# Kernel optimization log

Hardware: AMD Instinct MI355X
Metric: run time of the kernel (lower is better)

Reference implementation:

```python
import jax, jax.numpy as jnp
import numpy as np

N_NODES = 100000
N_EDGES = 1600000
IN_DIM, HID_DIM, OUT_DIM = 256, 64, 64


def gcn_conv(x, W, b, row, col, ew):
    """PyG GCNConv: linear transform, add self-loops (weight 1), symmetric
    deg^{-1/2} normalization, gather-scale-scatter_add aggregation, bias."""
    n = x.shape[0]
    x = x @ W  # [N, out]
    loops = jnp.arange(n)
    row_f = jnp.concatenate([row, loops])
    col_f = jnp.concatenate([col, loops])
    ew_f = jnp.concatenate([ew, jnp.ones((n,), x.dtype)])
    deg = jax.ops.segment_sum(ew_f, col_f, num_segments=n)  # [N]
    dinv = jnp.where(deg > 0, jax.lax.rsqrt(deg), jnp.zeros_like(deg))
    norm = dinv[row_f] * ew_f * dinv[col_f]  # [E+N]
    msg = x[row_f] * norm[:, None]  # gather + scale, [E+N, out]
    out = jax.ops.segment_sum(msg, col_f, num_segments=n)  # scatter-add
    return out + b


def setup_inputs() -> dict:
    key = jax.random.key(0)
    k1, k2, k3, k4, k5 = jax.random.split(key, 5)
    x = jax.random.normal(k1, (N_NODES, IN_DIM), dtype=jnp.float32)
    edge_index = jax.random.randint(k2, (2, N_EDGES), 0, N_NODES, dtype=jnp.int64)
    edge_count = jax.random.randint(k3, (N_EDGES, 1), 0, 1000, dtype=jnp.int64)
    W1 = jax.random.normal(k4, (IN_DIM, HID_DIM), dtype=jnp.float32) * (1.0 / np.sqrt(IN_DIM))
    b1 = jnp.zeros((HID_DIM,), jnp.float32)
    W2 = jax.random.normal(k5, (HID_DIM, OUT_DIM), dtype=jnp.float32) * (1.0 / np.sqrt(HID_DIM))
    b2 = jnp.zeros((OUT_DIM,), jnp.float32)
    return {"x": x, "edge_index": edge_index, "edge_count": edge_count,
            "W1": W1, "b1": b1, "W2": W2, "b2": b2}


def reference(x, edge_index, edge_count, W1, b1, W2, b2):
    # edge weight: min-max normalize edge_count (squeezed)
    ec = edge_count[:, 0].astype(jnp.float32)
    ew = (ec - ec.min()) / (ec.max() - ec.min())
    row, col = edge_index[0], edge_index[1]
    h = jax.nn.relu(gcn_conv(x, W1, b1, row, col, ew))
    h = gcn_conv(h, W2, b2, row, col, ew)
    # dropout(p=0.5) is identity in eval mode
    node_embeddings = h
    return node_embeddings, jax.nn.log_softmax(h, axis=-1)
```

## Files before the change

### kernel.cpp

```cpp
#include <hip/hip_runtime.h>
#include <climits>

#define CNT_SHIFT 20
#define SUM_MASK  ((1u << 20) - 1)
#define ROW_BITS 17
#define ROW_MASK ((1u << ROW_BITS) - 1)
#define MAXDEG 64
#define HIST_ILP 4

__device__ __forceinline__ unsigned short f2bf(float f) {
  unsigned u = __float_as_uint(f);
  u = (u + 0x7fffu + ((u >> 16) & 1u)) >> 16;
  return (unsigned short)u;
}
__device__ __forceinline__ float bf_lo(unsigned d) { return __uint_as_float(d << 16); }
__device__ __forceinline__ float bf_hi(unsigned d) { return __uint_as_float(d & 0xffff0000u); }

__device__ __forceinline__ void gload16(const float* g, float* l) {
  __builtin_amdgcn_global_load_lds(
      (const __attribute__((address_space(1))) void*)(g),
      (__attribute__((address_space(3))) void*)(l),
      16, 0, 0);
}

__global__ __launch_bounds__(256) void k_mega(
    const float* __restrict__ A, const float* __restrict__ W,
    unsigned short* __restrict__ outh, int nN,
    const int* __restrict__ erow, const int* __restrict__ ecol,
    const int* __restrict__ ec,
    unsigned* __restrict__ packed, unsigned* __restrict__ srcw2,
    int* __restrict__ mm, int nE, int Bg, int S, int stride) {
  __shared__ float atile[128 * 32];
  __shared__ float wtile[32 * 64];
  __shared__ int sred[8];
  const int bid = blockIdx.x;
  const bool slot = (bid % S) == 0;
  const int kq = bid / S;

  if (slot && kq < Bg) {
    constexpr int K = 256, KSTEPS = K / 32;
    const int tid = threadIdx.x;
    const int wv = tid >> 6;
    const int tr = tid >> 4, tc = tid & 15;
    const int rbase = kq * 128;

    float4 acc[8];
    #pragma unroll
    for (int i = 0; i < 8; ++i) acc[i] = make_float4(0.f, 0.f, 0.f, 0.f);

    for (int kt = 0; kt < KSTEPS; ++kt) {
      #pragma unroll
      for (int r = 0; r < 4; ++r) {
        int f = r * 256 + tid;
        int row = f >> 3, c4s = f & 7;
        int c4 = c4s ^ (row & 7);
        int gr = rbase + row; if (gr >= nN) gr = nN - 1;
        gload16(A + (size_t)gr * K + kt * 32 + c4 * 4,
                &atile[(r * 256 + wv * 64) * 4]);
      }
      #pragma unroll
      for (int r = 0; r < 2; ++r) {
        int f = r * 256 + tid;
        int krow = f >> 4, c4 = f & 15;
        gload16(W + (size_t)(kt * 32 + krow) * 64 + c4 * 4,
                &wtile[(r * 256 + wv * 64) * 4]);
      }
      __syncthreads();
      #pragma unroll
      for (int k4 = 0; k4 < 8; ++k4) {
        float4 wv0 = *(const float4*)&wtile[(k4 * 4 + 0) * 64 + tc * 4];
        float4 wv1 = *(const float4*)&wtile[(k4 * 4 + 1) * 64 + tc * 4];
        float4 wv2 = *(const float4*)&wtile[(k4 * 4 + 2) * 64 + tc * 4];
        float4 wv3 = *(const float4*)&wtile[(k4 * 4 + 3) * 64 + tc * 4];
        #pragma unroll
        for (int i = 0; i < 8; ++i) {
          int row = tr + 16 * i;
          float4 av = *(const float4*)&atile[row * 32 + ((k4 ^ (row & 7)) * 4)];
          acc[i].x = fmaf(av.x, wv0.x, acc[i].x);
          acc[i].y = fmaf(av.x, wv0.y, acc[i].y);
          acc[i].z = fmaf(av.x, wv0.z, acc[i].z);
          acc[i].w = fmaf(av.x, wv0.w, acc[i].w);
          acc[i].x = fmaf(av.y, wv1.x, acc[i].x);
          acc[i].y = fmaf(av.y, wv1.y, acc[i].y);
          acc[i].z = fmaf(av.y, wv1.z, acc[i].z);
          acc[i].w = fmaf(av.y, wv1.w, acc[i].w);
          acc[i].x = fmaf(av.z, wv2.x, acc[i].x);
          acc[i].y = fmaf(av.z, wv2.y, acc[i].y);
          acc[i].z = fmaf(av.z, wv2.z, acc[i].z);
          acc[i].w = fmaf(av.z, wv2.w, acc[i].w);
          acc[i].x = fmaf(av.w, wv3.x, acc[i].x);
          acc[i].y = fmaf(av.w, wv3.y, acc[i].y);
          acc[i].z = fmaf(av.w, wv3.z, acc[i].z);
          acc[i].w = fmaf(av.w, wv3.w, acc[i].w);
        }
      }
      __syncthreads();
    }
    #pragma unroll
    for (int i = 0; i < 8; ++i) {
      int row = rbase + tr + 16 * i;
      if (row < nN) {
        ushort4 o4;
        o4.x = f2bf(acc[i].x); o4.y = f2bf(acc[i].y);
        o4.z = f2bf(acc[i].z); o4.w = f2bf(acc[i].w);
        *(ushort4*)&outh[(size_t)row * 64 + tc * 4] = o4;
      }
    }
    return;
  }

  int ng = slot ? min(kq, Bg) : min(kq + 1, Bg);
  int h = bid - ng;
  int gid = h * 256 + threadIdx.x;
  int vmin = INT_MAX, vmax = INT_MIN;
  #pragma unroll
  for (int k = 0; k < HIST_ILP; ++k) {
    int e = gid + k * stride;
    if (e < nE) {
      int w = ec[e];
      int c = ecol[e];
      vmin = min(vmin, w); vmax = max(vmax, w);
      unsigned old = atomicAdd(&packed[c], (1u << CNT_SHIFT) | (unsigned)w);
      int rk = (int)(old >> CNT_SHIFT); if (rk > MAXDEG - 1) rk = MAXDEG - 1;
      srcw2[(size_t)c * MAXDEG + rk] = (unsigned)erow[e] | ((unsigned)w << ROW_BITS);
    }
  }
  #pragma unroll
  for (int o = 32; o > 0; o >>= 1) {
    vmin = min(vmin, __shfl_xor(vmin, o));
    vmax = max(vmax, __shfl_xor(vmax, o));
  }
  int wid = threadIdx.x >> 6;
  if ((threadIdx.x & 63) == 0) { sred[wid] = vmin; sred[4 + wid] = vmax; }
  __syncthreads();
  if (threadIdx.x == 0) {
    #pragma unroll
    for (int w2 = 1; w2 < 4; ++w2) {
      vmin = min(vmin, sred[w2]);
      vmax = max(vmax, sred[4 + w2]);
    }
    if (vmin != INT_MAX) atomicMax(&mm[0], 0x7FFFFFFF - vmin);
    if (vmax != INT_MIN) atomicMax(&mm[1], vmax);
  }
}

__global__ void k_dinv(const unsigned* __restrict__ packed,
                       const int* __restrict__ mm,
                       float* __restrict__ dinv, int n) {
  int i = blockIdx.x * blockDim.x + threadIdx.x;
  if (i >= n) return;
  unsigned pk = packed[i];
  int v = (int)(pk >> CNT_SHIFT);
  float mn = (float)(0x7FFFFFFF - mm[0]);
  float rcp = 1.0f / ((float)mm[1] - mn);
  float deg = ((float)(pk & SUM_MASK) - (float)v * mn) * rcp;
  dinv[i] = rsqrtf(deg + 1.0f);
}

__global__ __launch_bounds__(256) void k_gemm64(const float* __restrict__ A,
                                                const float* __restrict__ W,
                                                unsigned short* __restrict__ outh,
                                                int n) {
  constexpr int K = 64, KSTEPS = K / 32;
  __shared__ float atile[2][128 * 32];
  __shared__ float wtile[2][32 * 64];
  const int tid = threadIdx.x;
  const int wv = tid >> 6;
  const int tr = tid >> 4, tc = tid & 15;
  const int rbase = blockIdx.x * 128;

  auto stageA = [&](int kt, int b) {
    #pragma unroll
    for (int r = 0; r < 4; ++r) {
      int f = r * 256 + tid;
      int row = f >> 3, c4s = f & 7;
      int c4 = c4s ^ (row & 7);
      int gr = rbase + row; if (gr >= n) gr = n - 1;
      gload16(A + (size_t)gr * K + kt * 32 + c4 * 4,
              &atile[b][(r * 256 + wv * 64) * 4]);
    }
  };
  auto stageW = [&](int kt, int b) {
    #pragma unroll
    for (int r = 0; r < 2; ++r) {
      int f = r * 256 + tid;
      int krow = f >> 4, c4 = f & 15;
      gload16(W + (size_t)(kt * 32 + krow) * 64 + c4 * 4,
              &wtile[b][(r * 256 + wv * 64) * 4]);
    }
  };

  float4 acc[8];
  #pragma unroll
  for (int i = 0; i < 8; ++i) acc[i] = make_float4(0.f, 0.f, 0.f, 0.f);

  stageA(0, 0); stageW(0, 0);
  __syncthreads();
  int cur = 0;
  for (int kt = 0; kt < KSTEPS; ++kt) {
    if (kt + 1 < KSTEPS) { stageA(kt + 1, cur ^ 1); stageW(kt + 1, cur ^ 1); }
    const float* ab = atile[cur];
    const float* wb = wtile[cur];
    #pragma unroll
    for (int k4 = 0; k4 < 8; ++k4) {
      float4 wv0 = *(const float4*)&wb[(k4 * 4 + 0) * 64 + tc * 4];
      float4 wv1 = *(const float4*)&wb[(k4 * 4 + 1) * 64 + tc * 4];
      float4 wv2 = *(const float4*)&wb[(k4 * 4 + 2) * 64 + tc * 4];
      float4 wv3 = *(const float4*)&wb[(k4 * 4 + 3) * 64 + tc * 4];
      #pragma unroll
      for (int i = 0; i < 8; ++i) {
        int row = tr + 16 * i;
        float4 av = *(const float4*)&ab[row * 32 + ((k4 ^ (row & 7)) * 4)];
        acc[i].x = fmaf(av.x, wv0.x, acc[i].x);
        acc[i].y = fmaf(av.x, wv0.y, acc[i].y);
        acc[i].z = fmaf(av.x, wv0.z, acc[i].z);
        acc[i].w = fmaf(av.x, wv0.w, acc[i].w);
        acc[i].x = fmaf(av.y, wv1.x, acc[i].x);
        acc[i].y = fmaf(av.y, wv1.y, acc[i].y);
        acc[i].z = fmaf(av.y, wv1.z, acc[i].z);
        acc[i].w = fmaf(av.y, wv1.w, acc[i].w);
        acc[i].x = fmaf(av.z, wv2.x, acc[i].x);
        acc[i].y = fmaf(av.z, wv2.y, acc[i].y);
        acc[i].z = fmaf(av.z, wv2.z, acc[i].z);
        acc[i].w = fmaf(av.z, wv2.w, acc[i].w);
        acc[i].x = fmaf(av.w, wv3.x, acc[i].x);
        acc[i].y = fmaf(av.w, wv3.y, acc[i].y);
        acc[i].z = fmaf(av.w, wv3.z, acc[i].z);
        acc[i].w = fmaf(av.w, wv3.w, acc[i].w);
      }
    }
    __syncthreads();
    cur ^= 1;
  }
  #pragma unroll
  for (int i = 0; i < 8; ++i) {
    int row = rbase + tr + 16 * i;
    if (row < n) {
      ushort4 o4;
      o4.x = f2bf(acc[i].x); o4.y = f2bf(acc[i].y);
      o4.z = f2bf(acc[i].z); o4.w = f2bf(acc[i].w);
      *(ushort4*)&outh[(size_t)row * 64 + tc * 4] = o4;
    }
  }
}

template<bool FINAL>
__global__ void k_agg(const unsigned* __restrict__ packed,
                      const unsigned* __restrict__ srcw2,
                      const int* __restrict__ mm,
                      const float* __restrict__ dinv,
                      const unsigned short* __restrict__ xwh,
                      const float* __restrict__ b,
                      float* __restrict__ outp, int nN) {
  int node = blockIdx.x * (blockDim.x >> 6) + (threadIdx.x >> 6);
  if (node >= nN) return;
  int lane = threadIdx.x & 63;
  int grp = lane >> 3, sub = lane & 7;
  float mn = (float)(0x7FFFFFFF - mm[0]);
  float rcp = 1.0f / ((float)mm[1] - mn);
  float dc = dinv[node];
  const uint4* xw16 = (const uint4*)xwh;
  float acc[8] = {0.f, 0.f, 0.f, 0.f, 0.f, 0.f, 0.f, 0.f};
  size_t s = (size_t)node * MAXDEG;
  int m = min((int)(packed[node] >> CNT_SHIFT), MAXDEG);
  {
    int take = m;
    int rsrc = 0;
    float nrmv = 0.f;
    if (lane < take) {
      unsigned rw = srcw2[s + lane];
      rsrc = rw & ROW_MASK;
      nrmv = dinv[rsrc] * (((float)(rw >> ROW_BITS) - mn) * rcp) * dc;
    }
    for (int j = 0; j < take; j += 8) {
      int jj = j + grp;
      int r = __shfl(rsrc, jj);
      float nv = __shfl(nrmv, jj);
      uint4 d = xw16[(size_t)r * 8 + sub];
      acc[0] = fmaf(nv, bf_lo(d.x), acc[0]);
      acc[1] = fmaf(nv, bf_hi(d.x), acc[1]);
      acc[2] = fmaf(nv, bf_lo(d.y), acc[2]);
      acc[3] = fmaf(nv, bf_hi(d.y), acc[3]);
      acc[4] = fmaf(nv, bf_lo(d.z), acc[4]);
      acc[5] = fmaf(nv, bf_hi(d.z), acc[5]);
      acc[6] = fmaf(nv, bf_lo(d.w), acc[6]);
      acc[7] = fmaf(nv, bf_hi(d.w), acc[7]);
    }
  }
  #pragma unroll
  for (int k = 0; k < 8; ++k) acc[k] += __shfl_xor(acc[k], 8);
  #pragma unroll
  for (int k = 0; k < 8; ++k) acc[k] += __shfl_xor(acc[k], 16);
  #pragma unroll
  for (int k = 0; k < 8; ++k) acc[k] += __shfl_xor(acc[k], 32);

  if (lane < 8) {
    uint4 d = xw16[(size_t)node * 8 + sub];
    float sv[8] = {bf_lo(d.x), bf_hi(d.x), bf_lo(d.y), bf_hi(d.y),
                   bf_lo(d.z), bf_hi(d.z), bf_lo(d.w), bf_hi(d.w)};
    float dcc = dc * dc;
    float v[8];
    #pragma unroll
    for (int k = 0; k < 8; ++k) v[k] = acc[k] + dcc * sv[k] + b[sub * 8 + k];
    size_t o0 = (size_t)node * 64 + sub * 8;
    if (FINAL) {
      *(float4*)&outp[o0]     = make_float4(v[0], v[1], v[2], v[3]);
      *(float4*)&outp[o0 + 4] = make_float4(v[4], v[5], v[6], v[7]);
      float mx = v[0];
      #pragma unroll
      for (int k = 1; k < 8; ++k) mx = fmaxf(mx, v[k]);
      #pragma unroll
      for (int o = 1; o < 8; o <<= 1) mx = fmaxf(mx, __shfl_xor(mx, o));
      float e = 0.f;
      #pragma unroll
      for (int k = 0; k < 8; ++k) e += expf(v[k] - mx);
      #pragma unroll
      for (int o = 1; o < 8; o <<= 1) e += __shfl_xor(e, o);
      float ls = mx + logf(e);
      size_t o1 = (size_t)nN * 64 + o0;
      *(float4*)&outp[o1]     = make_float4(v[0] - ls, v[1] - ls, v[2] - ls, v[3] - ls);
      *(float4*)&outp[o1 + 4] = make_float4(v[4] - ls, v[5] - ls, v[6] - ls, v[7] - ls);
    } else {
      #pragma unroll
      for (int k = 0; k < 8; ++k) v[k] = fmaxf(v[k], 0.f);
      *(float4*)&outp[o0]     = make_float4(v[0], v[1], v[2], v[3]);
      *(float4*)&outp[o0 + 4] = make_float4(v[4], v[5], v[6], v[7]);
    }
  }
}

extern "C" void kernel_launch(void* const* d_in, const int* in_sizes, int n_in,
                              void* d_out, int out_size, void* d_ws, size_t ws_size,
                              hipStream_t stream) {
  const float* x  = (const float*)d_in[0];
  const int*   ei = (const int*)d_in[1];
  const int*   ec = (const int*)d_in[2];
  const float* W1 = (const float*)d_in[3];
  const float* b1 = (const float*)d_in[4];
  const float* W2 = (const float*)d_in[5];
  const float* b2 = (const float*)d_in[6];

  int nN = in_sizes[0] / 256;
  int nE = in_sizes[2];
  const int* erow = ei;
  const int* ecol = ei + nE;
  int n64 = nN * 64;

  auto al4 = [](size_t v) { return (v + 3) & ~(size_t)3; };
  int* wsi = (int*)d_ws;
  int* mm = wsi;
  size_t off = 16;
  unsigned* packed = (unsigned*)(wsi + off);          off = al4(off + (size_t)nN);
  float* dinv   = (float*)(wsi + off);                off = al4(off + nN);
  unsigned* srcw2 = (unsigned*)(wsi + off);           off = al4(off + (size_t)MAXDEG * nN);
  unsigned short* xwh = (unsigned short*)(wsi + off); off = al4(off + 32 * (size_t)nN);
  float* h1     = (float*)(wsi + off);                off = al4(off + (size_t)n64);
  float* outp   = (float*)d_out;

  hipMemsetAsync(d_ws, 0, (size_t)(16 + nN) * 4, stream);

  int Bg = (nN + 127) / 128;
  int Bh = (nE + 256 * HIST_ILP - 1) / (256 * HIST_ILP);
  int T  = Bg + Bh;
  int S  = T / Bg; if (S < 1) S = 1;
  k_mega<<<T, 256, 0, stream>>>(x, W1, xwh, nN, erow, ecol, ec, packed, srcw2,
                                mm, nE, Bg, S, Bh * 256);
  k_dinv<<<(nN + 255) / 256, 256, 0, stream>>>(packed, mm, dinv, nN);

  k_agg<false><<<(nN + 3) / 4, 256, 0, stream>>>(packed, srcw2, mm, dinv, xwh, b1, h1, nN);

  k_gemm64<<<Bg, 256, 0, stream>>>(h1, W2, xwh, nN);
  k_agg<true><<<(nN + 3) / 4, 256, 0, stream>>>(packed, srcw2, mm, dinv, xwh, b2, outp, nN);
}
```

Measured before the change: 243.7 us.

## Fuse layer-1 aggregation with layer-2 GEMM, dropping the h1 round trip

New measurement: 288.1 us. 18.2% more time.

```diff
diff --git a/kernel.cpp b/kernel.cpp
--- a/kernel.cpp
+++ b/kernel.cpp
@@ -157,101 +157,97 @@
   dinv[i] = rsqrtf(deg + 1.0f);
 }
 
-__global__ __launch_bounds__(256) void k_gemm64(const float* __restrict__ A,
-                                                const float* __restrict__ W,
-                                                unsigned short* __restrict__ outh,
-                                                int n) {
-  constexpr int K = 64, KSTEPS = K / 32;
-  __shared__ float atile[2][128 * 32];
-  __shared__ float wtile[2][32 * 64];
-  const int tid = threadIdx.x;
-  const int wv = tid >> 6;
-  const int tr = tid >> 4, tc = tid & 15;
-  const int rbase = blockIdx.x * 128;
-
-  auto stageA = [&](int kt, int b) {
-    #pragma unroll
-    for (int r = 0; r < 4; ++r) {
-      int f = r * 256 + tid;
-      int row = f >> 3, c4s = f & 7;
-      int c4 = c4s ^ (row & 7);
-      int gr = rbase + row; if (gr >= n) gr = n - 1;
-      gload16(A + (size_t)gr * K + kt * 32 + c4 * 4,
-              &atile[b][(r * 256 + wv * 64) * 4]);
-    }
-  };
-  auto stageW = [&](int kt, int b) {
-    #pragma unroll
-    for (int r = 0; r < 2; ++r) {
-      int f = r * 256 + tid;
-      int krow = f >> 4, c4 = f & 15;
-      gload16(W + (size_t)(kt * 32 + krow) * 64 + c4 * 4,
-              &wtile[b][(r * 256 + wv * 64) * 4]);
-    }
-  };
-
-  float4 acc[8];
-  #pragma unroll
-  for (int i = 0; i < 8; ++i) acc[i] = make_float4(0.f, 0.f, 0.f, 0.f);
-
-  stageA(0, 0); stageW(0, 0);
+__global__ __launch_bounds__(256) void k_aggg(
+    const unsigned* __restrict__ packed,
+    const unsigned* __restrict__ srcw2,
+    const int* __restrict__ mm,
+    const float* __restrict__ dinv,
+    const unsigned short* __restrict__ xwh,
+    const float* __restrict__ b1,
+    const float* __restrict__ W2,
+    unsigned short* __restrict__ outh,
+    int nN) {
+  __shared__ float wlds[64 * 64];
+  {
+    const float4* W4 = (const float4*)W2;
+    float4* wl4 = (float4*)wlds;
+    for (int i = threadIdx.x; i < 1024; i += 256) wl4[i] = W4[i];
+  }
   __syncthreads();
-  int cur = 0;
-  for (int kt = 0; kt < KSTEPS; ++kt) {
-    if (kt + 1 < KSTEPS) { stageA(kt + 1, cur ^ 1); stageW(kt + 1, cur ^ 1); }
-    const float* ab = atile[cur];
-    const float* wb = wtile[cur];
-    #pragma unroll
-    for (int k4 = 0; k4 < 8; ++k4) {
-      float4 wv0 = *(const float4*)&wb[(k4 * 4 + 0) * 64 + tc * 4];
-      float4 wv1 = *(const float4*)&wb[(k4 * 4 + 1) * 64 + tc * 4];
-      float4 wv2 = *(const float4*)&wb[(k4 * 4 + 2) * 64 + tc * 4];
-      float4 wv3 = *(const float4*)&wb[(k4 * 4 + 3) * 64 + tc * 4];
-      #pragma unroll
-      for (int i = 0; i < 8; ++i) {
-        int row = tr + 16 * i;
-        float4 av = *(const float4*)&ab[row * 32 + ((k4 ^ (row & 7)) * 4)];
-        acc[i].x = fmaf(av.x, wv0.x, acc[i].x);
-        acc[i].y = fmaf(av.x, wv0.y, acc[i].y);
-        acc[i].z = fmaf(av.x, wv0.z, acc[i].z);
-        acc[i].w = fmaf(av.x, wv0.w, acc[i].w);
-        acc[i].x = fmaf(av.y, wv1.x, acc[i].x);
-        acc[i].y = fmaf(av.y, wv1.y, acc[i].y);
-        acc[i].z = fmaf(av.y, wv1.z, acc[i].z);
-        acc[i].w = fmaf(av.y, wv1.w, acc[i].w);
-        acc[i].x = fmaf(av.z, wv2.x, acc[i].x);
-        acc[i].y = fmaf(av.z, wv2.y, acc[i].y);
-        acc[i].z = fmaf(av.z, wv2.z, acc[i].z);
-        acc[i].w = fmaf(av.z, wv2.w, acc[i].w);
-        acc[i].x = fmaf(av.w, wv3.x, acc[i].x);
-        acc[i].y = fmaf(av.w, wv3.y, acc[i].y);
-        acc[i].z = fmaf(av.w, wv3.z, acc[i].z);
-        acc[i].w = fmaf(av.w, wv3.w, acc[i].w);
-      }
-    }
-    __syncthreads();
-    cur ^= 1;
-  }
-  #pragma unroll
-  for (int i = 0; i < 8; ++i) {
-    int row = rbase + tr + 16 * i;
-    if (row < n) {
-      ushort4 o4;
-      o4.x = f2bf(acc[i].x); o4.y = f2bf(acc[i].y);
-      o4.z = f2bf(acc[i].z); o4.w = f2bf(acc[i].w);
-      *(ushort4*)&outh[(size_t)row * 64 + tc * 4] = o4;
-    }
-  }
-}
-
-template<bool FINAL>
-__global__ void k_agg(const unsigned* __restrict__ packed,
-                      const unsigned* __restrict__ srcw2,
-                      const int* __restrict__ mm,
-                      const float* __restrict__ dinv,
-                      const unsigned short* __restrict__ xwh,
-                      const float* __restrict__ b,
-                      float* __restrict__ outp, int nN) {
+  int wid = threadIdx.x >> 6, lane = threadIdx.x & 63;
+  int grp = lane >> 3, sub = lane & 7;
+  float mn = (float)(0x7FFFFFFF - mm[0]);
+  float rcp = 1.0f / ((float)mm[1] - mn);
+  const uint4* xw16 = (const uint4*)xwh;
+  float4 bv0 = ((const float4*)b1)[sub * 2];
+  float4 bv1 = ((const float4*)b1)[sub * 2 + 1];
+
+  for (int it = 0; it < 4; ++it) {
+    int node = blockIdx.x * 16 + it * 4 + wid;
+    if (node >= nN) return;
+    float dc = dinv[node];
+    float acc[8] = {0.f, 0.f, 0.f, 0.f, 0.f, 0.f, 0.f, 0.f};
+    size_t s = (size_t)node * MAXDEG;
+    int m = min((int)(packed[node] >> CNT_SHIFT), MAXDEG);
+    {
+      int rsrc = 0;
+      float nrmv = 0.f;
+      if (lane < m) {
+        unsigned rw = srcw2[s + lane];
+        rsrc = rw & ROW_MASK;
+        nrmv = dinv[rsrc] * (((float)(rw >> ROW_BITS) - mn) * rcp) * dc;
+      }
+      for (int j = 0; j < m; j += 8) {
+        int jj = j + grp;
+        int r = __shfl(rsrc, jj);
+        float nv = __shfl(nrmv, jj);
+        uint4 d = xw16[(size_t)r * 8 + sub];
+        acc[0] = fmaf(nv, bf_lo(d.x), acc[0]);
+        acc[1] = fmaf(nv, bf_hi(d.x), acc[1]);
+        acc[2] = fmaf(nv, bf_lo(d.y), acc[2]);
+        acc[3] = fmaf(nv, bf_hi(d.y), acc[3]);
+        acc[4] = fmaf(nv, bf_lo(d.z), acc[4]);
+        acc[5] = fmaf(nv, bf_hi(d.z), acc[5]);
+        acc[6] = fmaf(nv, bf_lo(d.w), acc[6]);
+        acc[7] = fmaf(nv, bf_hi(d.w), acc[7]);
+      }
+    }
+    #pragma unroll
+    for (int k = 0; k < 8; ++k) acc[k] += __shfl_xor(acc[k], 8);
+    #pragma unroll
+    for (int k = 0; k < 8; ++k) acc[k] += __shfl_xor(acc[k], 16);
+    #pragma unroll
+    for (int k = 0; k < 8; ++k) acc[k] += __shfl_xor(acc[k], 32);
+
+    uint4 d = xw16[(size_t)node * 8 + sub];
+    float sv[8] = {bf_lo(d.x), bf_hi(d.x), bf_lo(d.y), bf_hi(d.y),
+                   bf_lo(d.z), bf_hi(d.z), bf_lo(d.w), bf_hi(d.w)};
+    float dcc = dc * dc;
+    float v[8];
+    v[0] = fmaxf(acc[0] + dcc * sv[0] + bv0.x, 0.f);
+    v[1] = fmaxf(acc[1] + dcc * sv[1] + bv0.y, 0.f);
+    v[2] = fmaxf(acc[2] + dcc * sv[2] + bv0.z, 0.f);
+    v[3] = fmaxf(acc[3] + dcc * sv[3] + bv0.w, 0.f);
+    v[4] = fmaxf(acc[4] + dcc * sv[4] + bv1.x, 0.f);
+    v[5] = fmaxf(acc[5] + dcc * sv[5] + bv1.y, 0.f);
+    v[6] = fmaxf(acc[6] + dcc * sv[6] + bv1.z, 0.f);
+    v[7] = fmaxf(acc[7] + dcc * sv[7] + bv1.w, 0.f);
+
+    float og = 0.f;
+    #pragma unroll
+    for (int k = 0; k < 64; ++k)
+      og = fmaf(__shfl(v[k & 7], k >> 3), wlds[k * 64 + lane], og);
+    outh[(size_t)node * 64 + lane] = f2bf(og);
+  }
+}
+
+__global__ void k_agg2(const unsigned* __restrict__ packed,
+                       const unsigned* __restrict__ srcw2,
+                       const int* __restrict__ mm,
+                       const float* __restrict__ dinv,
+                       const unsigned short* __restrict__ xwh,
+                       const float* __restrict__ b,
+                       float* __restrict__ outp, int nN) {
   int node = blockIdx.x * (blockDim.x >> 6) + (threadIdx.x >> 6);
   if (node >= nN) return;
   int lane = threadIdx.x & 63;
@@ -264,15 +260,14 @@
   size_t s = (size_t)node * MAXDEG;
   int m = min((int)(packed[node] >> CNT_SHIFT), MAXDEG);
   {
-    int take = m;
     int rsrc = 0;
     float nrmv = 0.f;
-    if (lane < take) {
+    if (lane < m) {
       unsigned rw = srcw2[s + lane];
       rsrc = rw & ROW_MASK;
       nrmv = dinv[rsrc] * (((float)(rw >> ROW_BITS) - mn) * rcp) * dc;
     }
-    for (int j = 0; j < take; j += 8) {
+    for (int j = 0; j < m; j += 8) {
       int jj = j + grp;
       int r = __shfl(rsrc, jj);
       float nv = __shfl(nrmv, jj);
@@ -303,29 +298,22 @@
     #pragma unroll
     for (int k = 0; k < 8; ++k) v[k] = acc[k] + dcc * sv[k] + b[sub * 8 + k];
     size_t o0 = (size_t)node * 64 + sub * 8;
-    if (FINAL) {
-      *(float4*)&outp[o0]     = make_float4(v[0], v[1], v[2], v[3]);
-      *(float4*)&outp[o0 + 4] = make_float4(v[4], v[5], v[6], v[7]);
-      float mx = v[0];
-      #pragma unroll
-      for (int k = 1; k < 8; ++k) mx = fmaxf(mx, v[k]);
-      #pragma unroll
-      for (int o = 1; o < 8; o <<= 1) mx = fmaxf(mx, __shfl_xor(mx, o));
-      float e = 0.f;
-      #pragma unroll
-      for (int k = 0; k < 8; ++k) e += expf(v[k] - mx);
-      #pragma unroll
-      for (int o = 1; o < 8; o <<= 1) e += __shfl_xor(e, o);
-      float ls = mx + logf(e);
-      size_t o1 = (size_t)nN * 64 + o0;
-      *(float4*)&outp[o1]     = make_float4(v[0] - ls, v[1] - ls, v[2] - ls, v[3] - ls);
-      *(float4*)&outp[o1 + 4] = make_float4(v[4] - ls, v[5] - ls, v[6] - ls, v[7] - ls);
-    } else {
-      #pragma unroll
-      for (int k = 0; k < 8; ++k) v[k] = fmaxf(v[k], 0.f);
-      *(float4*)&outp[o0]     = make_float4(v[0], v[1], v[2], v[3]);
-      *(float4*)&outp[o0 + 4] = make_float4(v[4], v[5], v[6], v[7]);
-    }
+    *(float4*)&outp[o0]     = make_float4(v[0], v[1], v[2], v[3]);
+    *(float4*)&outp[o0 + 4] = make_float4(v[4], v[5], v[6], v[7]);
+    float mx = v[0];
+    #pragma unroll
+    for (int k = 1; k < 8; ++k) mx = fmaxf(mx, v[k]);
+    #pragma unroll
+    for (int o = 1; o < 8; o <<= 1) mx = fmaxf(mx, __shfl_xor(mx, o));
+    float e = 0.f;
+    #pragma unroll
+    for (int k = 0; k < 8; ++k) e += expf(v[k] - mx);
+    #pragma unroll
+    for (int o = 1; o < 8; o <<= 1) e += __shfl_xor(e, o);
+    float ls = mx + logf(e);
+    size_t o1 = (size_t)nN * 64 + o0;
+    *(float4*)&outp[o1]     = make_float4(v[0] - ls, v[1] - ls, v[2] - ls, v[3] - ls);
+    *(float4*)&outp[o1 + 4] = make_float4(v[4] - ls, v[5] - ls, v[6] - ls, v[7] - ls);
   }
 }
 
@@ -344,17 +332,16 @@
   int nE = in_sizes[2];
   const int* erow = ei;
   const int* ecol = ei + nE;
-  int n64 = nN * 64;
 
   auto al4 = [](size_t v) { return (v + 3) & ~(size_t)3; };
   int* wsi = (int*)d_ws;
   int* mm = wsi;
   size_t off = 16;
-  unsigned* packed = (unsigned*)(wsi + off);          off = al4(off + (size_t)nN);
-  float* dinv   = (float*)(wsi + off);                off = al4(off + nN);
-  unsigned* srcw2 = (unsigned*)(wsi + off);           off = al4(off + (size_t)MAXDEG * nN);
-  unsigned short* xwh = (unsigned short*)(wsi + off); off = al4(off + 32 * (size_t)nN);
-  float* h1     = (float*)(wsi + off);                off = al4(off + (size_t)n64);
+  unsigned* packed = (unsigned*)(wsi + off);           off = al4(off + (size_t)nN);
+  float* dinv   = (float*)(wsi + off);                 off = al4(off + nN);
+  unsigned* srcw2 = (unsigned*)(wsi + off);            off = al4(off + (size_t)MAXDEG * nN);
+  unsigned short* xwh  = (unsigned short*)(wsi + off); off = al4(off + 32 * (size_t)nN);
+  unsigned short* xwh2 = (unsigned short*)(wsi + off); off = al4(off + 32 * (size_t)nN);
   float* outp   = (float*)d_out;
 
   hipMemsetAsync(d_ws, 0, (size_t)(16 + nN) * 4, stream);
@@ -367,8 +354,8 @@
                                 mm, nE, Bg, S, Bh * 256);
   k_dinv<<<(nN + 255) / 256, 256, 0, stream>>>(packed, mm, dinv, nN);
 
-  k_agg<false><<<(nN + 3) / 4, 256, 0, stream>>>(packed, srcw2, mm, dinv, xwh, b1, h1, nN);
-
-  k_gemm64<<<Bg, 256, 0, stream>>>(h1, W2, xwh, nN);
-  k_agg<true><<<(nN + 3) / 4, 256, 0, stream>>>(packed, srcw2, mm, dinv, xwh, b2, outp, nN);
-}
+  k_aggg<<<(nN + 15) / 16, 256, 0, stream>>>(packed, srcw2, mm, dinv, xwh, b1,
+                                             W2, xwh2, nN);
+
+  k_agg2<<<(nN + 3) / 4, 256, 0, stream>>>(packed, srcw2, mm, dinv, xwh2, b2, outp, nN);
+}
```
